# Optimization experiments

Measured on AMD Instinct MI355X. Metric: run time of the kernel, lower is better.

Reference implementation:

```python
import jax, jax.numpy as jnp
import numpy as np

NUM_HEAD = 8


def setup_inputs() -> dict:
    key = jax.random.key(0)
    k1, k2, k3 = jax.random.split(key, 3)
    B, C, H, W = 8, 512, 32, 32
    x = jax.random.normal(k1, (B, C, H, W), dtype=jnp.float32)
    # 1x1 conv weights stored as plain matrices (out_ch, in_ch)
    Wqkv = jax.random.normal(k2, (3 * C, C), dtype=jnp.float32) * (1.0 / np.sqrt(C))
    Wo = jax.random.normal(k3, (C, C), dtype=jnp.float32) * (1.0 / np.sqrt(C))
    bo = jnp.zeros((C,), dtype=jnp.float32)
    return {"x": x, "Wqkv": Wqkv, "Wo": Wo, "bo": bo}


def reference(x, Wqkv, Wo, bo):
    B, C, H, W = x.shape
    nh = NUM_HEAD
    d = C // nh
    S = H * W
    scale = 1.0 / np.sqrt(d)
    # 1x1 conv == channel matmul: (B,3C,H,W)
    x_ = jnp.einsum('bchw,oc->bohw', x, Wqkv)
    # reshape to (B, nh, 3d, H, W) and chunk along dim 2 (matches torch chunk order)
    qkv = x_.reshape(B, nh, 3 * d, H, W)
    q, k, v = qkv[:, :, :d], qkv[:, :, d:2 * d], qkv[:, :, 2 * d:]
    # flatten heads into batch, spatial into sequence
    q = q.reshape(B * nh, d, S).transpose(0, 2, 1) * scale  # (BH, S, d)
    k = k.reshape(B * nh, d, S)                             # (BH, d, S)
    v = v.reshape(B * nh, d, S).transpose(0, 2, 1)          # (BH, S, d)
    attn = jax.nn.softmax(jnp.matmul(q, k), axis=-1)        # (BH, S, S)
    out = jnp.matmul(attn, v)                               # (BH, S, d)
    result = out.transpose(0, 2, 1).reshape(B, C, H, W)
    # output 1x1 conv with bias + residual
    y = jnp.einsum('bchw,oc->bohw', result, Wo) + bo[None, :, None, None]
    return y + x
```

## Files before the change

kernel.cpp:

```cpp
#include <hip/hip_runtime.h>
#include <hip/hip_bf16.h>

#define C_DIM 512
#define S_DIM 1024
#define NH 8
#define HD 64

typedef __attribute__((ext_vector_type(8))) short bf16x8;
typedef __attribute__((ext_vector_type(8))) unsigned short u16x8;
typedef __attribute__((ext_vector_type(4))) unsigned short u16x4;
typedef __attribute__((ext_vector_type(4))) float f32x4;

__device__ __forceinline__ unsigned short f2b_hw(float f) {
  __hip_bfloat16 h = __float2bfloat16(f);
  return __builtin_bit_cast(unsigned short, h);
}

__device__ __forceinline__ f32x4 mfma16(bf16x8 a, bf16x8 b, f32x4 c) {
  return __builtin_amdgcn_mfma_f32_16x16x32_bf16(a, b, c, 0, 0, 0);
}

__device__ __forceinline__ void gload_lds16(const unsigned short* g, unsigned short* l) {
  __builtin_amdgcn_global_load_lds(
      (const __attribute__((address_space(1))) unsigned int*)g,
      (__attribute__((address_space(3))) unsigned int*)l, 16, 0, 0);
}

__global__ __launch_bounds__(256) void prep(
    const float* __restrict__ x, const float* __restrict__ Wqkv,
    const float* __restrict__ Wo,
    unsigned short* __restrict__ WqkvB, unsigned short* __restrict__ WoB,
    unsigned short* __restrict__ xT)
{
  __shared__ float T[64][65];
  const int bid = blockIdx.x;
  if (bid < 1024) {
    const int i = bid * 256 + threadIdx.x;
    const float* src;
    unsigned short* dst;
    int off;
    float mul = 1.0f;
    if (i < 196608) {
      src = Wqkv; dst = WqkvB; off = i * 4;
      const int o = off >> 9;
      if ((o % 192) < 64) mul = 0.18033688011112042f;
    } else {
      src = Wo; dst = WoB; off = (i - 196608) * 4;
    }
    const float4 v = *(const float4*)(src + off);
    const u16x4 pk = {f2b_hw(v.x * mul), f2b_hw(v.y * mul),
                      f2b_hw(v.z * mul), f2b_hw(v.w * mul)};
    *(u16x4*)(dst + off) = pk;
  } else {
    const int idx = bid - 1024;
    const int st = idx & 15, ct = (idx >> 4) & 7, b = idx >> 7;
    const int c0 = ct * 64, s0 = st * 64;
    const int tr = threadIdx.x >> 4, tc4 = (threadIdx.x & 15) * 4;
#pragma unroll
    for (int rep = 0; rep < 4; ++rep) {
      const int c = rep * 16 + tr;
      *(float4*)&T[c][tc4] =
          *(const float4*)(x + ((size_t)(b * C_DIM + c0 + c)) * S_DIM + s0 + tc4);
    }
    __syncthreads();
#pragma unroll
    for (int rep = 0; rep < 4; ++rep) {
      const int s = rep * 16 + tr;
      const u16x4 pk = {f2b_hw(T[tc4 + 0][s]), f2b_hw(T[tc4 + 1][s]),
                        f2b_hw(T[tc4 + 2][s]), f2b_hw(T[tc4 + 3][s])};
      *(u16x4*)(xT + ((size_t)(b * S_DIM + s0 + s)) * C_DIM + c0 + tc4) = pk;
    }
  }
}

__global__ __launch_bounds__(256) void proj_qkv(
    const unsigned short* __restrict__ A, const unsigned short* __restrict__ Bm,
    unsigned short* __restrict__ Q, unsigned short* __restrict__ K,
    unsigned short* __restrict__ Vt)
{
  const int b = blockIdx.z, ot = blockIdx.y, st = blockIdx.x;
  const int o0 = ot * 128, s0 = st * 128;
  const int tid = threadIdx.x;
  const int w = tid >> 6, lane = tid & 63;
  const int g = lane >> 4, j16 = lane & 15;
  const int wr = w >> 1, wc = w & 1;

  __shared__ __align__(16) unsigned short lds[2048 * 8];
  char* const Al = (char*)lds;
  char* const Bl = (char*)lds + 16384;

  f32x4 acc[4][4];
#pragma unroll
  for (int mt = 0; mt < 4; ++mt)
#pragma unroll
    for (int nt = 0; nt < 4; ++nt) {
      acc[mt][nt].x = 0.f; acc[mt][nt].y = 0.f;
      acc[mt][nt].z = 0.f; acc[mt][nt].w = 0.f;
    }

  for (int k0 = 0; k0 < C_DIM; k0 += 64) {
    __syncthreads();
#pragma unroll
    for (int it = 0; it < 8; ++it) {
      const int chunk = it * 256 + tid;
      const int cid = chunk & 1023;
      const int row = cid >> 3;
      const int colb = (cid & 7) << 4;
      const int srcb = colb ^ ((row & 7) << 4);
      const unsigned short* gp;
      if (it < 4) gp = A + (size_t)(o0 + row) * C_DIM + k0 + (srcb >> 1);
      else        gp = Bm + ((size_t)(b * S_DIM) + s0 + row) * C_DIM + k0 + (srcb >> 1);
      gload_lds16(gp, lds + (size_t)(it * 256 + w * 64) * 8);
    }
    __syncthreads();

#pragma unroll
    for (int ks = 0; ks < 2; ++ks) {
      bf16x8 af[4], bfr[4];
#pragma unroll
      for (int mt = 0; mt < 4; ++mt) {
        const int r = wr * 64 + mt * 16 + j16;
        af[mt] = __builtin_bit_cast(
            bf16x8, *(const u16x8*)(Al + r * 128 + ((ks * 64 + g * 16) ^ ((r & 7) << 4))));
      }
#pragma unroll
      for (int nt = 0; nt < 4; ++nt) {
        const int r = wc * 64 + nt * 16 + j16;
        bfr[nt] = __builtin_bit_cast(
            bf16x8, *(const u16x8*)(Bl + r * 128 + ((ks * 64 + g * 16) ^ ((r & 7) << 4))));
      }
#pragma unroll
      for (int mt = 0; mt < 4; ++mt)
#pragma unroll
        for (int nt = 0; nt < 4; ++nt)
          acc[mt][nt] = mfma16(af[mt], bfr[nt], acc[mt][nt]);
    }
  }

#pragma unroll
  for (int mt = 0; mt < 4; ++mt) {
    const int ob = o0 + wr * 64 + mt * 16 + g * 4;
    const int head = ob / 192, type = (ob % 192) >> 6, d = ob & 63;
    const int bh = b * NH + head;
    if (type < 2) {
      unsigned short* const dst = (type == 0) ? Q : K;
#pragma unroll
      for (int nt = 0; nt < 4; ++nt) {
        const int s = s0 + wc * 64 + nt * 16 + j16;
        const f32x4 a = acc[mt][nt];
        const u16x4 pk = {f2b_hw(a.x), f2b_hw(a.y), f2b_hw(a.z), f2b_hw(a.w)};
        *(u16x4*)(dst + ((size_t)bh * S_DIM + s) * HD + d) = pk;
      }
    } else {
#pragma unroll
      for (int nt = 0; nt < 4; ++nt) {
        const int spos = nt * 16 + j16;
        const int p = (spos & 35) | ((spos & 12) << 1) | ((spos & 16) >> 2);
        const size_t col = (size_t)(s0 + wc * 64 + p);
        const f32x4 a = acc[mt][nt];
#pragma unroll
        for (int q = 0; q < 4; ++q)
          Vt[((size_t)bh * HD + d + q) * S_DIM + col] = f2b_hw(a[q]);
      }
    }
  }
}

__global__ __launch_bounds__(256) void proj_out(
    const unsigned short* __restrict__ A, const unsigned short* __restrict__ Bm,
    float* __restrict__ y, const float* __restrict__ bo,
    const float* __restrict__ resid)
{
  const int b = blockIdx.z, ot = blockIdx.y, st = blockIdx.x;
  const int o0 = ot * 64, s0 = st * 128;
  const int tid = threadIdx.x;
  const int w = tid >> 6, lane = tid & 63;
  const int g = lane >> 4, j16 = lane & 15;

  __shared__ __align__(16) unsigned short lds[1536 * 8];
  char* const Al = (char*)lds;
  char* const Bl = (char*)lds + 8192;

  f32x4 acc[4][2];
#pragma unroll
  for (int mt = 0; mt < 4; ++mt)
#pragma unroll
    for (int nt = 0; nt < 2; ++nt) {
      acc[mt][nt].x = 0.f; acc[mt][nt].y = 0.f;
      acc[mt][nt].z = 0.f; acc[mt][nt].w = 0.f;
    }

  for (int k0 = 0; k0 < C_DIM; k0 += 64) {
    __syncthreads();
#pragma unroll
    for (int it = 0; it < 6; ++it) {
      const int cid = (it < 2) ? (it * 256 + tid) : ((it - 2) * 256 + tid);
      const int row = cid >> 3;
      const int srcb = ((cid & 7) << 4) ^ ((row & 7) << 4);
      if (it < 2) {
        gload_lds16(A + (size_t)(o0 + row) * C_DIM + k0 + (srcb >> 1),
                    lds + (size_t)(it * 256 + w * 64) * 8);
      } else {
        gload_lds16(Bm + ((size_t)(b * S_DIM) + s0 + row) * C_DIM + k0 + (srcb >> 1),
                    lds + (size_t)(512 + (it - 2) * 256 + w * 64) * 8);
      }
    }
    __syncthreads();

#pragma unroll
    for (int ks = 0; ks < 2; ++ks) {
      bf16x8 af[4], bfr[2];
#pragma unroll
      for (int mt = 0; mt < 4; ++mt) {
        const int r = mt * 16 + j16;
        af[mt] = __builtin_bit_cast(
            bf16x8, *(const u16x8*)(Al + r * 128 + ((ks * 64 + g * 16) ^ ((r & 7) << 4))));
      }
#pragma unroll
      for (int nt = 0; nt < 2; ++nt) {
        const int r = w * 32 + nt * 16 + j16;
        bfr[nt] = __builtin_bit_cast(
            bf16x8, *(const u16x8*)(Bl + r * 128 + ((ks * 64 + g * 16) ^ ((r & 7) << 4))));
      }
#pragma unroll
      for (int mt = 0; mt < 4; ++mt)
#pragma unroll
        for (int nt = 0; nt < 2; ++nt)
          acc[mt][nt] = mfma16(af[mt], bfr[nt], acc[mt][nt]);
    }
  }

#pragma unroll
  for (int mt = 0; mt < 4; ++mt) {
    const int ob = o0 + mt * 16 + g * 4;
#pragma unroll
    for (int nt = 0; nt < 2; ++nt) {
      const int s = s0 + w * 32 + nt * 16 + j16;
#pragma unroll
      for (int q = 0; q < 4; ++q) {
        const int o = ob + q;
        const size_t idx = ((size_t)(b * C_DIM + o)) * S_DIM + s;
        y[idx] = acc[mt][nt][q] + bo[o] + resid[idx];
      }
    }
  }
}

__global__ __launch_bounds__(512) void attn_mfma(
    const unsigned short* __restrict__ Qg, const unsigned short* __restrict__ Kg,
    const unsigned short* __restrict__ Vg, unsigned short* __restrict__ AOt)
{
  const int bh = blockIdx.x;
  const int qb = blockIdx.y;
  const int b = bh >> 3, head = bh & 7;
  const int tid = threadIdx.x;
  const int w = tid >> 6, lane = tid & 63;
  const int g = lane >> 4, j16 = lane & 15;
  const int qw0 = qb * 128 + w * 16;

  __shared__ __align__(16) unsigned short KV[3][2][4096];

  bf16x8 qf[2];
#pragma unroll
  for (int ks = 0; ks < 2; ++ks)
    qf[ks] = __builtin_bit_cast(
        bf16x8, *(const u16x8*)(Qg + ((size_t)bh * S_DIM + qw0 + j16) * HD +
                                ks * 32 + g * 8));

  auto STAGE = [&](int buf, int k0) {
    const int cid = tid;
    const int row = cid >> 3;
    const int srcb = ((cid & 7) << 4) ^ ((row & 7) << 4);
    unsigned short* const dst = &KV[buf][0][0] + (size_t)(w * 64) * 8;
    gload_lds16(Kg + ((size_t)bh * S_DIM + k0 + row) * HD + (srcb >> 1), dst);
    gload_lds16(Vg + ((size_t)bh * HD + row) * S_DIM + k0 + (srcb >> 1), dst + 4096);
  };

  f32x4 oacc[4];
#pragma unroll
  for (int mt = 0; mt < 4; ++mt) {
    oacc[mt].x = 0.f; oacc[mt].y = 0.f; oacc[mt].z = 0.f; oacc[mt].w = 0.f;
  }
  float lsum = 0.f;

  STAGE(0, 0);
  STAGE(1, 64);

  for (int kt = 0; kt < 16; ++kt) {
    if (kt < 15) asm volatile("s_waitcnt vmcnt(2)" ::: "memory");
    else         asm volatile("s_waitcnt vmcnt(0)" ::: "memory");
    __builtin_amdgcn_s_barrier();
    if (kt < 14) STAGE((kt + 2) % 3, (kt + 2) * 64);

    const char* const Kl = (const char*)KV + (kt % 3) * 16384;
    const char* const Vl = Kl + 8192;

    f32x4 sacc[4];
    __builtin_amdgcn_s_setprio(1);
#pragma unroll
    for (int mt = 0; mt < 4; ++mt) {
      const int row = mt * 16 + j16;
      const int sw = (row & 7) << 4;
      const bf16x8 kf0 = __builtin_bit_cast(
          bf16x8, *(const u16x8*)(Kl + row * 128 + ((g * 16) ^ sw)));
      f32x4 z; z.x = 0.f; z.y = 0.f; z.z = 0.f; z.w = 0.f;
      sacc[mt] = mfma16(kf0, qf[0], z);
      const bf16x8 kf1 = __builtin_bit_cast(
          bf16x8, *(const u16x8*)(Kl + row * 128 + ((64 + g * 16) ^ sw)));
      sacc[mt] = mfma16(kf1, qf[1], sacc[mt]);
    }
    __builtin_amdgcn_s_setprio(0);

    u16x4 pf4[4];
#pragma unroll
    for (int mt = 0; mt < 4; ++mt) {
      f32x4 p;
      p.x = exp2f(sacc[mt].x);
      p.y = exp2f(sacc[mt].y);
      p.z = exp2f(sacc[mt].z);
      p.w = exp2f(sacc[mt].w);
      lsum += (p.x + p.y) + (p.z + p.w);
      pf4[mt] = u16x4{f2b_hw(p.x), f2b_hw(p.y), f2b_hw(p.z), f2b_hw(p.w)};
    }

    __builtin_amdgcn_s_setprio(1);
#pragma unroll
    for (int ks = 0; ks < 2; ++ks) {
      const bf16x8 pfr = __builtin_bit_cast(
          bf16x8, __builtin_shufflevector(pf4[2 * ks], pf4[2 * ks + 1],
                                          0, 1, 2, 3, 4, 5, 6, 7));
#pragma unroll
      for (int mt = 0; mt < 4; ++mt) {
        const int row = mt * 16 + j16;
        const int sw = (row & 7) << 4;
        const bf16x8 vf = __builtin_bit_cast(
            bf16x8, *(const u16x8*)(Vl + row * 128 + ((ks * 64 + g * 16) ^ sw)));
        oacc[mt] = mfma16(vf, pfr, oacc[mt]);
      }
    }
    __builtin_amdgcn_s_setprio(0);
  }

  lsum += __shfl_xor(lsum, 16);
  lsum += __shfl_xor(lsum, 32);
  const float rl = 1.f / lsum;

  const int q = qw0 + j16;
#pragma unroll
  for (int mt = 0; mt < 4; ++mt) {
    const f32x4 a = oacc[mt];
    const u16x4 pk = {f2b_hw(a.x * rl), f2b_hw(a.y * rl), f2b_hw(a.z * rl), f2b_hw(a.w * rl)};
    *(u16x4*)(AOt + ((size_t)(b * S_DIM + q)) * C_DIM + head * HD + mt * 16 + g * 4) = pk;
  }
}

extern "C" void kernel_launch(void* const* d_in, const int* in_sizes, int n_in,
                              void* d_out, int out_size, void* d_ws, size_t ws_size,
                              hipStream_t stream) {
  const float* x    = (const float*)d_in[0];
  const float* Wqkv = (const float*)d_in[1];
  const float* Wo   = (const float*)d_in[2];
  const float* bo   = (const float*)d_in[3];
  float* y = (float*)d_out;

  unsigned short* WqkvB = (unsigned short*)d_ws;
  unsigned short* WoB   = WqkvB + 786432;
  unsigned short* xT    = WoB + 262144;
  unsigned short* Q     = xT + 4194304;
  unsigned short* K     = Q + 4194304;
  unsigned short* Vt    = K + 4194304;
  unsigned short* AOt   = Vt + 4194304;

  prep<<<dim3(2048), 256, 0, stream>>>(x, Wqkv, Wo, WqkvB, WoB, xT);
  proj_qkv<<<dim3(8, 12, 8), 256, 0, stream>>>(WqkvB, xT, Q, K, Vt);
  attn_mfma<<<dim3(64, 8), 512, 0, stream>>>(Q, K, Vt, AOt);
  proj_out<<<dim3(8, 8, 8), 256, 0, stream>>>(WoB, AOt, y, bo, x);
}
```

Baseline: 78.44 us.

## Software-pipeline attention loop to overlap next QK^T with current PV

Restructures the attention key loop so the QK^T MFMAs for tile i+1 are issued alongside the PV MFMAs for tile i, with the exp/bf16 conversion of tile i done before that block. The loop is unrolled by two with ping-pong score registers, an extra barrier is added around K/V staging, and launch bounds now request 4 blocks per CU. The aim is to hide the latency of the exp2 softmax stage behind matrix work. In exchange it raises register pressure and adds a barrier per iteration.

```diff
diff --git a/kernel.cpp b/kernel.cpp
--- a/kernel.cpp
+++ b/kernel.cpp
@@ -246,7 +246,7 @@
   }
 }
 
-__global__ __launch_bounds__(512) void attn_mfma(
+__global__ __launch_bounds__(512, 4) void attn_mfma(
     const unsigned short* __restrict__ Qg, const unsigned short* __restrict__ Kg,
     const unsigned short* __restrict__ Vg, unsigned short* __restrict__ AOt)
 {
@@ -276,27 +276,8 @@
     gload_lds16(Vg + ((size_t)bh * HD + row) * S_DIM + k0 + (srcb >> 1), dst + 4096);
   };
 
-  f32x4 oacc[4];
-#pragma unroll
-  for (int mt = 0; mt < 4; ++mt) {
-    oacc[mt].x = 0.f; oacc[mt].y = 0.f; oacc[mt].z = 0.f; oacc[mt].w = 0.f;
-  }
-  float lsum = 0.f;
-
-  STAGE(0, 0);
-  STAGE(1, 64);
-
-  for (int kt = 0; kt < 16; ++kt) {
-    if (kt < 15) asm volatile("s_waitcnt vmcnt(2)" ::: "memory");
-    else         asm volatile("s_waitcnt vmcnt(0)" ::: "memory");
-    __builtin_amdgcn_s_barrier();
-    if (kt < 14) STAGE((kt + 2) % 3, (kt + 2) * 64);
-
-    const char* const Kl = (const char*)KV + (kt % 3) * 16384;
-    const char* const Vl = Kl + 8192;
-
-    f32x4 sacc[4];
-    __builtin_amdgcn_s_setprio(1);
+  auto QKT = [&](int KT, f32x4 (&S)[4]) {
+    const char* const Kl = (const char*)KV + (KT % 3) * 16384;
 #pragma unroll
     for (int mt = 0; mt < 4; ++mt) {
       const int row = mt * 16 + j16;
@@ -304,26 +285,22 @@
       const bf16x8 kf0 = __builtin_bit_cast(
           bf16x8, *(const u16x8*)(Kl + row * 128 + ((g * 16) ^ sw)));
       f32x4 z; z.x = 0.f; z.y = 0.f; z.z = 0.f; z.w = 0.f;
-      sacc[mt] = mfma16(kf0, qf[0], z);
+      S[mt] = mfma16(kf0, qf[0], z);
       const bf16x8 kf1 = __builtin_bit_cast(
           bf16x8, *(const u16x8*)(Kl + row * 128 + ((64 + g * 16) ^ sw)));
-      sacc[mt] = mfma16(kf1, qf[1], sacc[mt]);
-    }
-    __builtin_amdgcn_s_setprio(0);
-
-    u16x4 pf4[4];
-#pragma unroll
-    for (int mt = 0; mt < 4; ++mt) {
-      f32x4 p;
-      p.x = exp2f(sacc[mt].x);
-      p.y = exp2f(sacc[mt].y);
-      p.z = exp2f(sacc[mt].z);
-      p.w = exp2f(sacc[mt].w);
-      lsum += (p.x + p.y) + (p.z + p.w);
-      pf4[mt] = u16x4{f2b_hw(p.x), f2b_hw(p.y), f2b_hw(p.z), f2b_hw(p.w)};
-    }
-
-    __builtin_amdgcn_s_setprio(1);
+      S[mt] = mfma16(kf1, qf[1], S[mt]);
+    }
+  };
+
+  f32x4 oacc[4];
+#pragma unroll
+  for (int mt = 0; mt < 4; ++mt) {
+    oacc[mt].x = 0.f; oacc[mt].y = 0.f; oacc[mt].z = 0.f; oacc[mt].w = 0.f;
+  }
+  float lsum = 0.f;
+
+  auto PV = [&](int I, const u16x4 (&pf4)[4]) {
+    const char* const Vl = (const char*)KV + (I % 3) * 16384 + 8192;
 #pragma unroll
     for (int ks = 0; ks < 2; ++ks) {
       const bf16x8 pfr = __builtin_bit_cast(
@@ -338,8 +315,62 @@
         oacc[mt] = mfma16(vf, pfr, oacc[mt]);
       }
     }
+  };
+
+  f32x4 sA[4], sB[4];
+
+  STAGE(0, 0);
+  STAGE(1, 64);
+  asm volatile("s_waitcnt vmcnt(2)" ::: "memory");
+  __builtin_amdgcn_s_barrier();
+  QKT(0, sA);
+
+#define ATTN_BODY(I, SCUR, SNXT)                                               \
+  {                                                                            \
+    u16x4 pf4[4];                                                              \
+    _Pragma("unroll")                                                          \
+    for (int mt = 0; mt < 4; ++mt) {                                           \
+      f32x4 p;                                                                 \
+      p.x = exp2f(SCUR[mt].x);                                                 \
+      p.y = exp2f(SCUR[mt].y);                                                 \
+      p.z = exp2f(SCUR[mt].z);                                                 \
+      p.w = exp2f(SCUR[mt].w);                                                 \
+      lsum += (p.x + p.y) + (p.z + p.w);                                       \
+      pf4[mt] = u16x4{f2b_hw(p.x), f2b_hw(p.y), f2b_hw(p.z), f2b_hw(p.w)};     \
+    }                                                                          \
+    __builtin_amdgcn_s_barrier();   \
+    if ((I) + 2 <= 15) STAGE(((I) + 2) % 3, ((I) + 2) * 64);                   \
+    if ((I) < 14) asm volatile("s_waitcnt vmcnt(2)" ::: "memory");             \
+    else          asm volatile("s_waitcnt vmcnt(0)" ::: "memory");             \
+    __builtin_amdgcn_s_barrier();           \
+    __builtin_amdgcn_s_setprio(1);                                             \
+    if ((I) < 15) QKT((I) + 1, SNXT);      \
+    PV((I), pf4);                                                              \
+    __builtin_amdgcn_s_setprio(0);                                             \
+  }
+
+  for (int ii = 0; ii < 7; ++ii) {
+    ATTN_BODY(2 * ii,     sA, sB)
+    ATTN_BODY(2 * ii + 1, sB, sA)
+  }
+  ATTN_BODY(14, sA, sB)
+  {
+    u16x4 pf4[4];
+#pragma unroll
+    for (int mt = 0; mt < 4; ++mt) {
+      f32x4 p;
+      p.x = exp2f(sB[mt].x);
+      p.y = exp2f(sB[mt].y);
+      p.z = exp2f(sB[mt].z);
+      p.w = exp2f(sB[mt].w);
+      lsum += (p.x + p.y) + (p.z + p.w);
+      pf4[mt] = u16x4{f2b_hw(p.x), f2b_hw(p.y), f2b_hw(p.z), f2b_hw(p.w)};
+    }
+    __builtin_amdgcn_s_setprio(1);
+    PV(15, pf4);
     __builtin_amdgcn_s_setprio(0);
   }
+#undef ATTN_BODY
 
   lsum += __shfl_xor(lsum, 16);
   lsum += __shfl_xor(lsum, 32);
```

Result: no change. 78.70 us (+0.3%).
